# Optimization experiments

Hardware: AMD Instinct MI355X
Metric: run time of the kernel (lower is better)

## Reference

```python
import jax, jax.numpy as jnp
import numpy as np

D_MODEL = 1024
NUM_HEADS = 16
BATCH = 2
SEQ = 2048


def _trunc_normal(key, shape, std):
    # truncated normal on [-3std, 3std], matching torch.nn.init.trunc_normal_
    return jax.random.truncated_normal(key, -3.0, 3.0, shape, dtype=jnp.float32) * std


def setup_inputs() -> dict:
    key = jax.random.key(0)
    kx, kq, kk, kv, ko = jax.random.split(key, 5)
    std = (2.0 / (D_MODEL + D_MODEL)) ** 0.5
    return {
        "X": jax.random.normal(kx, (BATCH, SEQ, D_MODEL), dtype=jnp.float32),
        "q_proj": _trunc_normal(kq, (D_MODEL, D_MODEL), std),
        "k_proj": _trunc_normal(kk, (D_MODEL, D_MODEL), std),
        "v_proj": _trunc_normal(kv, (D_MODEL, D_MODEL), std),
        "o_proj": _trunc_normal(ko, (D_MODEL, D_MODEL), std),
    }


def reference(X, q_proj, k_proj, v_proj, o_proj):
    B, S, D = X.shape
    H = NUM_HEADS
    d_k = D // H

    # weights stored as (d_model, d_model); split output dim into heads
    q_w = q_proj.reshape(H, d_k, D)        # heads d_k d_model
    k_w = k_proj.reshape(H, d_k, D)
    v_w = v_proj.reshape(H, d_k, D)
    o_w = o_proj.reshape(D, H, d_k).transpose(1, 0, 2)  # heads d_model d_v

    q = jnp.einsum('hkd,bsd->bhsk', q_w, X)  # [B,H,S,d_k]
    k = jnp.einsum('hkd,bsd->bhsk', k_w, X)
    v = jnp.einsum('hkd,bsd->bhsk', v_w, X)

    scale = 1.0 / jnp.sqrt(jnp.asarray(d_k, dtype=X.dtype))
    scores = jnp.einsum('bhqk,bhsk->bhqs', q, k) * scale  # [B,H,S,S]
    causal = jnp.tril(jnp.ones((S, S), dtype=bool))
    scores = jnp.where(causal, scores, jnp.asarray(-jnp.inf, dtype=scores.dtype))
    attn = jax.nn.softmax(scores, axis=-1)
    attn_out = jnp.einsum('bhqs,bhsk->bhqk', attn, v)  # [B,H,S,d_v]

    return jnp.einsum('hdv,bhsv->bsd', o_w, attn_out)  # [B,S,d_model]
```

## Files before the change

kernel.cpp:

```cpp
#include <hip/hip_runtime.h>

typedef unsigned short u16;
typedef unsigned u32;
typedef __bf16 bf16x8 __attribute__((ext_vector_type(8)));
typedef float f32x4 __attribute__((ext_vector_type(4)));
typedef u16 u16x8 __attribute__((ext_vector_type(8)));
typedef u16 u16x4v __attribute__((ext_vector_type(4)));

#define D_MODEL 1024
#define SEQ 2048
#define NB 2
#define NH 16

#define MFMA(a, b, c) __builtin_amdgcn_mfma_f32_16x16x32_bf16(a, b, c, 0, 0, 0)

__device__ __forceinline__ u16 f2bf(float f) {
  unsigned u = __builtin_bit_cast(unsigned, f);
  u += 0x7FFFu + ((u >> 16) & 1u);
  return (u16)(u >> 16);
}

__device__ __forceinline__ u16 f2bf_hw(float f) {
  return __builtin_bit_cast(u16, (__bf16)f);
}

__device__ __forceinline__ bf16x8 ld8(const u16* p) {
  return __builtin_bit_cast(bf16x8, *(const u16x8*)p);
}

typedef const __attribute__((address_space(1))) unsigned gu32;
typedef __attribute__((address_space(3))) unsigned lu32;
__device__ __forceinline__ void gload16(const u16* g, u16* l) {
  __builtin_amdgcn_global_load_lds((gu32*)g, (lu32*)l, 16, 0, 0);
}

#define WAITV8 asm volatile("s_waitcnt vmcnt(8)" ::: "memory")
#define WAITV4 asm volatile("s_waitcnt vmcnt(4)" ::: "memory")
#define WAITV0 asm volatile("s_waitcnt vmcnt(0)" ::: "memory")
#define BARRIER __builtin_amdgcn_s_barrier()
#define SB0 __builtin_amdgcn_sched_barrier(0)

__global__ __launch_bounds__(256) void convert_kernel(
    const float* __restrict__ X, const float* __restrict__ Wq,
    const float* __restrict__ Wk, const float* __restrict__ Wv,
    const float* __restrict__ Wo, u16* __restrict__ Xb, u16* __restrict__ Wb)
{
  const int NX4 = 1024 * 1024;
  const int NW4 = 256 * 1024;
  const int TOT = NX4 + 4 * NW4;
  for (int i = blockIdx.x * 256 + threadIdx.x; i < TOT; i += gridDim.x * 256) {
    const float* src;
    u16* dst;
    if (i < NX4) {
      src = X + (size_t)i * 4;
      dst = Xb + (size_t)i * 4;
    } else {
      int j = i - NX4;
      int w = j >> 18;
      int off = j & (NW4 - 1);
      const float* ws = (w == 0) ? Wq : (w == 1) ? Wk : (w == 2) ? Wv : Wo;
      src = ws + (size_t)off * 4;
      dst = Wb + (size_t)j * 4;
    }
    float4 v = *(const float4*)src;
    u16x4v o = { f2bf(v.x), f2bf(v.y), f2bf(v.z), f2bf(v.w) };
    *(u16x4v*)dst = o;
  }
}

__global__ __launch_bounds__(512, 2) void qkv8w(
    const u16* __restrict__ A, const u16* __restrict__ B,
    u16* __restrict__ Qb, u16* __restrict__ Kb, u16* __restrict__ Vt)
{
  __shared__ u16 As[4][8192];
  __shared__ u16 Bs[4][8192];
  const int t = threadIdx.x;
  const int lane = t & 63, w = t >> 6;
  const int wm = w >> 2, wn = w & 3;

  const int lid = blockIdx.x + 16 * blockIdx.y;
  const int xcd = lid & 7;
  const int k = lid >> 3;
  const int bx = (xcd >> 1) * 4 + (k & 3);
  const int by = (xcd & 1) * 6 + (k >> 2);

  const int m0 = bx * 256;
  const int kg = lane >> 4, lr = lane & 15;
  const int rp = lr >> 1, hf = lr & 1;
  const int xr = (((hf * 4 + kg) ^ rp) * 8);

  const int lc = (lane & 7) ^ (lane >> 3);
  const int ghalf = lc >> 2, kc = lc & 3;
  const int n0 = by * 256;

  f32x4 acc[8][4] = {};

  auto stage = [&](int buf, int kt) {
    #pragma unroll
    for (int j = 0; j < 2; ++j) {
      int g = (j * 64 + w * 8 + (lane >> 3)) * 2 + ghalf;
      gload16(&A[(size_t)(m0 + g) * 1024 + kt * 32 + kc * 8],
              &As[buf][(j * 8 + w) * 512]);
      gload16(&B[(size_t)(n0 + g) * 1024 + kt * 32 + kc * 8],
              &Bs[buf][(j * 8 + w) * 512]);
    }
  };

  auto phase = [&](int buf) {
    const u16* as = &As[buf][0];
    const u16* bs = &Bs[buf][0];
    bf16x8 a[8], b[4];
    #pragma unroll
    for (int mi = 0; mi < 8; ++mi)
      a[mi] = ld8(&as[(wm * 64 + mi * 8 + rp) * 64 + xr]);
    #pragma unroll
    for (int ni = 0; ni < 4; ++ni)
      b[ni] = ld8(&bs[(wn * 32 + ni * 8 + rp) * 64 + xr]);
    __builtin_amdgcn_s_setprio(1);
    #pragma unroll
    for (int mi = 0; mi < 8; ++mi)
      #pragma unroll
      for (int ni = 0; ni < 4; ++ni)
        acc[mi][ni] = MFMA(a[mi], b[ni], acc[mi][ni]);
    __builtin_amdgcn_s_setprio(0);
  };

  stage(0, 0);
  stage(1, 1);
  stage(2, 2);

  for (int tt = 0; tt < 28; tt += 4) {
    #pragma unroll
    for (int q = 0; q < 4; ++q) {
      const int kt = tt + q;
      WAITV8;
      BARRIER;
      SB0;
      stage((q + 3) & 3, kt + 3);
      phase(q);
    }
  }
  WAITV8; BARRIER; SB0; stage(3, 31); phase(0);
  WAITV8; BARRIER; SB0; phase(1);
  WAITV4; BARRIER; SB0; phase(2);
  WAITV0; BARRIER; SB0; phase(3);

  const int zby = by >> 2;
  const int nl0 = (by & 3) * 256;
  const float scl = (zby == 0) ? 0.125f : 1.0f;
  #pragma unroll
  for (int mi = 0; mi < 8; ++mi) {
    #pragma unroll
    for (int ni = 0; ni < 4; ++ni) {
      int m = m0 + wm * 128 + mi * 16 + kg * 4;
      int nl = nl0 + wn * 64 + ni * 16 + lr;
      int bb = m >> 11, s = m & (SEQ - 1);
      int h = nl >> 6, dk = nl & 63;
      size_t bh = (size_t)(bb * NH + h);
      if (zby == 2) {
        u16x4v v = { f2bf(acc[mi][ni][0]), f2bf(acc[mi][ni][1]),
                     f2bf(acc[mi][ni][2]), f2bf(acc[mi][ni][3]) };
        *(u16x4v*)&Vt[(bh * 64 + dk) * SEQ + s] = v;
      } else {
        u16* dst = (zby == 0 ? Qb : Kb) + ((bh * SEQ + s) * 64 + dk);
        #pragma unroll
        for (int i = 0; i < 4; ++i) dst[(size_t)i * 64] = f2bf(acc[mi][ni][i] * scl);
      }
    }
  }
}

__global__ __launch_bounds__(256) void oproj_kernel(
    const u16* __restrict__ A, const u16* __restrict__ B,
    float* __restrict__ out)
{
  __shared__ u16 As[2][128 * 64];
  __shared__ u16 Bs[2][128 * 64];
  const int t = threadIdx.x;
  const int lane = t & 63, w = t >> 6;
  const int wr = w >> 1, wc = w & 1;
  const int m0 = blockIdx.x * 128;
  const int n0 = blockIdx.y * 128;
  const int kg = lane >> 4, lr = lane & 15;
  const int lrow = lane >> 3, lch = lane & 7;

  f32x4 acc[4][4] = {};

  auto stage = [&](int buf, int kt) {
    #pragma unroll
    for (int i = 0; i < 4; ++i) {
      int row = (w * 4 + i) * 8 + lrow;
      int sch = lch ^ (row & 7);
      gload16(&A[(size_t)(m0 + row) * 1024 + kt * 64 + sch * 8], &As[buf][(w * 4 + i) * 512]);
      gload16(&B[(size_t)(n0 + row) * 1024 + kt * 64 + sch * 8], &Bs[buf][(w * 4 + i) * 512]);
    }
  };

  stage(0, 0);
  __syncthreads();
  int cur = 0;

  for (int kt = 0; kt < 16; ++kt) {
    if (kt + 1 < 16) stage(cur ^ 1, kt + 1);

    const u16* as = &As[cur][0];
    const u16* bs = &Bs[cur][0];
    #pragma unroll
    for (int kh = 0; kh < 2; ++kh) {
      bf16x8 a[4], b[4];
      #pragma unroll
      for (int mi = 0; mi < 4; ++mi) {
        int row = wr * 64 + mi * 16 + lr;
        int ch = (kh * 4 + kg) ^ (lr & 7);
        a[mi] = ld8(&as[row * 64 + ch * 8]);
      }
      #pragma unroll
      for (int ni = 0; ni < 4; ++ni) {
        int row = wc * 64 + ni * 16 + lr;
        int ch = (kh * 4 + kg) ^ (lr & 7);
        b[ni] = ld8(&bs[row * 64 + ch * 8]);
      }
      #pragma unroll
      for (int mi = 0; mi < 4; ++mi)
        #pragma unroll
        for (int ni = 0; ni < 4; ++ni)
          acc[mi][ni] = MFMA(a[mi], b[ni], acc[mi][ni]);
    }

    __syncthreads();
    cur ^= 1;
  }

  #pragma unroll
  for (int mi = 0; mi < 4; ++mi) {
    #pragma unroll
    for (int ni = 0; ni < 4; ++ni) {
      int m = m0 + wr * 64 + mi * 16 + kg * 4;
      int n = n0 + wc * 64 + ni * 16 + lr;
      #pragma unroll
      for (int i = 0; i < 4; ++i)
        out[(size_t)(m + i) * D_MODEL + n] = acc[mi][ni][i];
    }
  }
}

__global__ __launch_bounds__(256) void attn_kernel(
    const u16* __restrict__ Qb, const u16* __restrict__ Kb,
    const u16* __restrict__ Vt, u16* __restrict__ AO)
{
  __shared__ u16 Ks[2][64 * 64];
  __shared__ u16 Vs[2][64 * 64];
  __shared__ u16 Ps[4][16 * 64];
  const int t = threadIdx.x;
  const int bh = blockIdx.x;
  const int qt = 31 - blockIdx.y;
  const int lane = t & 63, wv = t >> 6;
  const int kg = lane >> 4, lr = lane & 15;
  const int r8 = lane >> 3, c = lane & 7;
  const int b = bh >> 4, h = bh & (NH - 1);

  auto stage = [&](int buf, int kv0) {
    #pragma unroll
    for (int i = 0; i < 2; ++i) {
      int s = wv * 2 + i;
      int row = s * 8 + r8;
      int sc = c ^ (row & 7);
      gload16(&Kb[((size_t)bh * SEQ + kv0 + row) * 64 + sc * 8], &Ks[buf][s * 512]);
      gload16(&Vt[((size_t)bh * 64 + row) * SEQ + kv0 + sc * 8], &Vs[buf][s * 512]);
    }
  };

  const int ntile = qt + 1;
  const int q0 = qt * 64;
  const int qg = q0 + wv * 16 + lr;

  const size_t qrow = (size_t)bh * SEQ + qg;
  bf16x8 aq0 = ld8(&Qb[qrow * 64 + kg * 8]);
  bf16x8 aq1 = ld8(&Qb[qrow * 64 + 32 + kg * 8]);

  f32x4 of[4] = {};
  float rs = 0.f;

  stage(0, 0);
  int cur = 0;
  u16* ps = &Ps[wv][0];
  const int pwr = lr * 64;
  const int ch0 = kg ^ (lr & 7);
  const int ch1 = (4 + kg) ^ (lr & 7);

  for (int kt = 0; kt < ntile; ++kt) {
    const int kv0 = kt * 64;
    __syncthreads();
    if (kt + 1 < ntile) stage(cur ^ 1, (kt + 1) * 64);

    const u16* kb = &Ks[cur][0];
    f32x4 sc4[4] = {};
    __builtin_amdgcn_s_setprio(1);
    #pragma unroll
    for (int ct = 0; ct < 4; ++ct) {
      sc4[ct] = MFMA(ld8(&kb[(ct * 16 + lr) * 64 + ch0 * 8]), aq0, sc4[ct]);
      sc4[ct] = MFMA(ld8(&kb[(ct * 16 + lr) * 64 + ch1 * 8]), aq1, sc4[ct]);
    }
    __builtin_amdgcn_s_setprio(0);

    const bool domask = (kt == ntile - 1);
    #pragma unroll
    for (int ct = 0; ct < 4; ++ct) {
      #pragma unroll
      for (int i = 0; i < 4; ++i) {
        float e = __expf(sc4[ct][i]);
        if (domask && (kv0 + ct * 16 + kg * 4 + i > qg)) e = 0.f;
        sc4[ct][i] = e;
        rs += e;
      }
      u16x4v pw = { f2bf_hw(sc4[ct][0]), f2bf_hw(sc4[ct][1]),
                    f2bf_hw(sc4[ct][2]), f2bf_hw(sc4[ct][3]) };
      *(u16x4v*)&ps[pwr + (((2 * ct + (kg >> 1)) ^ (lr & 7)) * 8 + (kg & 1) * 4)] = pw;
    }

    bf16x8 pa0 = ld8(&ps[pwr + ch0 * 8]);
    bf16x8 pa1 = ld8(&ps[pwr + ch1 * 8]);

    const u16* vb = &Vs[cur][0];
    __builtin_amdgcn_s_setprio(1);
    #pragma unroll
    for (int vt = 0; vt < 4; ++vt) {
      of[vt] = MFMA(pa0, ld8(&vb[(vt * 16 + lr) * 64 + ch0 * 8]), of[vt]);
      of[vt] = MFMA(pa1, ld8(&vb[(vt * 16 + lr) * 64 + ch1 * 8]), of[vt]);
    }
    __builtin_amdgcn_s_setprio(0);
    cur ^= 1;
  }

  rs += __shfl_xor(rs, 16, 64);
  rs += __shfl_xor(rs, 32, 64);

  #pragma unroll
  for (int i = 0; i < 4; ++i) {
    float inv = 1.0f / __shfl(rs, kg * 4 + i, 64);
    int s = q0 + wv * 16 + kg * 4 + i;
    size_t base = ((size_t)(b * SEQ + s)) * D_MODEL + h * 64 + lr;
    #pragma unroll
    for (int vt = 0; vt < 4; ++vt)
      AO[base + vt * 16] = f2bf_hw(of[vt][i] * inv);
  }
}

extern "C" void kernel_launch(void* const* d_in, const int* in_sizes, int n_in,
                              void* d_out, int out_size, void* d_ws, size_t ws_size,
                              hipStream_t stream) {
  const float* X  = (const float*)d_in[0];
  const float* Wq = (const float*)d_in[1];
  const float* Wk = (const float*)d_in[2];
  const float* Wv = (const float*)d_in[3];
  const float* Wo = (const float*)d_in[4];
  float* out = (float*)d_out;

  u16* Xb = (u16*)d_ws;
  u16* Wb = Xb + (size_t)4096 * 1024;
  u16* Qb = Wb + (size_t)4096 * 1024;
  u16* Kb = Qb + (size_t)4096 * 1024;
  u16* Vt = Kb + (size_t)4096 * 1024;
  u16* AO = Vt + (size_t)4096 * 1024;

  convert_kernel<<<2048, 256, 0, stream>>>(X, Wq, Wk, Wv, Wo, Xb, Wb);
  qkv8w<<<dim3(16, 12), 512, 0, stream>>>(Xb, Wb, Qb, Kb, Vt);
  attn_kernel<<<dim3(32, 32), 256, 0, stream>>>(Qb, Kb, Vt, AO);
  oproj_kernel<<<dim3(32, 8), 256, 0, stream>>>(AO, Wb + (size_t)3 * 1024 * 1024, out);
}
```

Measured before the change: 105.1 us.

## Restructure output projection GEMM to 8 waves with 4-stage async pipeline

Rewrites the output projection kernel to use 512 threads (8 waves in a 2x4 layout) with a 4-buffer shared-memory ring, prefetching three k-tiles ahead behind explicit vmcnt waits and barriers instead of a double buffer. It also raises wave priority around the MFMA bursts. The aim is to hide global-load latency and keep matrix units busy in this GEMM, at the cost of twice the LDS per block (64KB) and smaller per-wave tiles, which lowers register reuse.

New measurement: 99.20 us. -5.6%, faster.

```diff
diff --git a/kernel.cpp b/kernel.cpp
--- a/kernel.cpp
+++ b/kernel.cpp
@@ -170,78 +170,93 @@
   }
 }
 
-__global__ __launch_bounds__(256) void oproj_kernel(
+__global__ __launch_bounds__(512, 2) void oproj8w(
     const u16* __restrict__ A, const u16* __restrict__ B,
     float* __restrict__ out)
 {
-  __shared__ u16 As[2][128 * 64];
-  __shared__ u16 Bs[2][128 * 64];
+  __shared__ u16 As[4][8192];
+  __shared__ u16 Bs[4][8192];
   const int t = threadIdx.x;
   const int lane = t & 63, w = t >> 6;
-  const int wr = w >> 1, wc = w & 1;
+  const int wm = w >> 2, wn = w & 3;
   const int m0 = blockIdx.x * 128;
   const int n0 = blockIdx.y * 128;
   const int kg = lane >> 4, lr = lane & 15;
-  const int lrow = lane >> 3, lch = lane & 7;
-
-  f32x4 acc[4][4] = {};
+
+  const int srow = lane >> 3;
+  const int lc = (lane & 7) ^ srow;
+
+  f32x4 acc[4][2] = {};
 
   auto stage = [&](int buf, int kt) {
     #pragma unroll
-    for (int i = 0; i < 4; ++i) {
-      int row = (w * 4 + i) * 8 + lrow;
-      int sch = lch ^ (row & 7);
-      gload16(&A[(size_t)(m0 + row) * 1024 + kt * 64 + sch * 8], &As[buf][(w * 4 + i) * 512]);
-      gload16(&B[(size_t)(n0 + row) * 1024 + kt * 64 + sch * 8], &Bs[buf][(w * 4 + i) * 512]);
-    }
-  };
-
-  stage(0, 0);
-  __syncthreads();
-  int cur = 0;
-
-  for (int kt = 0; kt < 16; ++kt) {
-    if (kt + 1 < 16) stage(cur ^ 1, kt + 1);
-
-    const u16* as = &As[cur][0];
-    const u16* bs = &Bs[cur][0];
+    for (int j = 0; j < 2; ++j) {
+      int r = (j * 8 + w) * 8 + srow;
+      gload16(&A[(size_t)(m0 + r) * 1024 + kt * 64 + lc * 8],
+              &As[buf][(j * 8 + w) * 512]);
+      gload16(&B[(size_t)(n0 + r) * 1024 + kt * 64 + lc * 8],
+              &Bs[buf][(j * 8 + w) * 512]);
+    }
+  };
+
+  auto phase = [&](int buf) {
+    const u16* as = &As[buf][0];
+    const u16* bs = &Bs[buf][0];
     #pragma unroll
     for (int kh = 0; kh < 2; ++kh) {
-      bf16x8 a[4], b[4];
+      bf16x8 a[4], b[2];
       #pragma unroll
       for (int mi = 0; mi < 4; ++mi) {
-        int row = wr * 64 + mi * 16 + lr;
-        int ch = (kh * 4 + kg) ^ (lr & 7);
+        int row = wm * 64 + mi * 16 + lr;
+        int ch = (kh * 4 + kg) ^ (row & 7);
         a[mi] = ld8(&as[row * 64 + ch * 8]);
       }
       #pragma unroll
-      for (int ni = 0; ni < 4; ++ni) {
-        int row = wc * 64 + ni * 16 + lr;
-        int ch = (kh * 4 + kg) ^ (lr & 7);
+      for (int ni = 0; ni < 2; ++ni) {
+        int row = wn * 32 + ni * 16 + lr;
+        int ch = (kh * 4 + kg) ^ (row & 7);
         b[ni] = ld8(&bs[row * 64 + ch * 8]);
       }
+      __builtin_amdgcn_s_setprio(1);
       #pragma unroll
       for (int mi = 0; mi < 4; ++mi)
         #pragma unroll
-        for (int ni = 0; ni < 4; ++ni)
+        for (int ni = 0; ni < 2; ++ni)
           acc[mi][ni] = MFMA(a[mi], b[ni], acc[mi][ni]);
-    }
-
-    __syncthreads();
-    cur ^= 1;
-  }
+      __builtin_amdgcn_s_setprio(0);
+    }
+  };
+
+  stage(0, 0);
+  stage(1, 1);
+  stage(2, 2);
+
+  for (int tt = 0; tt < 12; tt += 4) {
+    #pragma unroll
+    for (int q = 0; q < 4; ++q) {
+      const int kt = tt + q;
+      WAITV8;
+      BARRIER;
+      SB0;
+      stage((q + 3) & 3, kt + 3);
+      phase(q);
+    }
+  }
+  WAITV8; BARRIER; SB0; stage(3, 15); phase(0);
+  WAITV8; BARRIER; SB0; phase(1);
+  WAITV4; BARRIER; SB0; phase(2);
+  WAITV0; BARRIER; SB0; phase(3);
 
   #pragma unroll
-  for (int mi = 0; mi < 4; ++mi) {
-    #pragma unroll
-    for (int ni = 0; ni < 4; ++ni) {
-      int m = m0 + wr * 64 + mi * 16 + kg * 4;
-      int n = n0 + wc * 64 + ni * 16 + lr;
+  for (int mi = 0; mi < 4; ++mi)
+    #pragma unroll
+    for (int ni = 0; ni < 2; ++ni) {
+      int m = m0 + wm * 64 + mi * 16 + kg * 4;
+      int n = n0 + wn * 32 + ni * 16 + lr;
       #pragma unroll
       for (int i = 0; i < 4; ++i)
         out[(size_t)(m + i) * D_MODEL + n] = acc[mi][ni][i];
     }
-  }
 }
 
 __global__ __launch_bounds__(256) void attn_kernel(
@@ -366,5 +381,5 @@
   convert_kernel<<<2048, 256, 0, stream>>>(X, Wq, Wk, Wv, Wo, Xb, Wb);
   qkv8w<<<dim3(16, 12), 512, 0, stream>>>(Xb, Wb, Qb, Kb, Vt);
   attn_kernel<<<dim3(32, 32), 256, 0, stream>>>(Qb, Kb, Vt, AO);
-  oproj_kernel<<<dim3(32, 8), 256, 0, stream>>>(AO, Wb + (size_t)3 * 1024 * 1024, out);
-}
+  oproj8w<<<dim3(32, 8), 512, 0, stream>>>(AO, Wb + (size_t)3 * 1024 * 1024, out);
+}
```
